# Performance work log

Measured on AMD Instinct MI355X. Metric: run time of the kernel, lower is better.

## Reference

```python
import jax, jax.numpy as jnp
import numpy as np

N, E, NS = 50000, 1600000, 25000
IN, HID, HEADS, EDIM = 5, 32, 4, 1
NEG_SLOPE = 0.2


def _gat(x, src, dst, ea, W, a_s, a_d, We, a_e, b, heads, out_ch, concat, n_nodes):
    # PyG GATConv (eval mode, dropout off): shared lin for src/dst, edge features fused.
    h = (x @ W).reshape(-1, heads, out_ch)               # [N, H, C]
    s_src = (h * a_s).sum(-1)                            # [N, H]
    s_dst = (h * a_d).sum(-1)                            # [N, H]
    he = (ea @ We).reshape(-1, heads, out_ch)            # [Ef, H, C]
    s_e = (he * a_e).sum(-1)                             # [Ef, H]
    logits = jax.nn.leaky_relu(s_src[src] + s_dst[dst] + s_e, NEG_SLOPE)  # [Ef, H]
    m = jax.ops.segment_max(logits, dst, num_segments=n_nodes)
    num = jnp.exp(logits - m[dst])
    den = jax.ops.segment_sum(num, dst, num_segments=n_nodes)
    alpha = num / (den[dst] + 1e-16)                     # per-dst softmax
    out = jax.ops.segment_sum(alpha[:, :, None] * h[src], dst, num_segments=n_nodes)
    out = out.reshape(n_nodes, heads * out_ch) if concat else out.mean(axis=1)
    return out + b, alpha


def setup_inputs():
    key = jax.random.key(0)
    ks = jax.random.split(key, 24)
    r = lambda i, shape: jax.random.normal(ks[i], shape, dtype=jnp.float32) * 0.1
    return dict(
        x=jax.random.normal(ks[0], (N, IN), dtype=jnp.float32),
        edge_attr=jax.random.normal(ks[1], (E, EDIM), dtype=jnp.float32),
        W1=r(2, (IN, HEADS * HID)), att_src1=r(3, (HEADS, HID)), att_dst1=r(4, (HEADS, HID)),
        We1=r(5, (EDIM, HEADS * HID)), att_e1=r(6, (HEADS, HID)), b1=jnp.zeros((HEADS * HID,), jnp.float32),
        W2=r(7, (HEADS * HID, HID)), att_src2=r(8, (1, HID)), att_dst2=r(9, (1, HID)),
        We2=r(10, (EDIM, HID)), att_e2=r(11, (1, HID)), b2=jnp.zeros((HID,), jnp.float32),
        Wa=r(12, (HID, 1)), ba=jnp.zeros((1,), jnp.float32),
        cash=jnp.zeros((1,), jnp.float32),
        Wc=r(13, (HID, 1)), bc=jnp.zeros((1,), jnp.float32),
        edge_index=jax.random.randint(ks[14], (2, E), 0, N),
        stock_idx=jnp.sort(jax.random.randint(ks[15], (NS,), 0, N)),
        batch=jnp.zeros((N,), jnp.int32),
    )


def reference(x, edge_attr, W1, att_src1, att_dst1, We1, att_e1, b1,
              W2, att_src2, att_dst2, We2, att_e2, b2,
              Wa, ba, cash, Wc, bc, edge_index, stock_idx, batch):
    src, dst = edge_index[0], edge_index[1]
    # add_self_loops with fill_value='mean' for edge_attr (PyG GATConv default)
    loop = jnp.arange(N, dtype=src.dtype)
    src_f = jnp.concatenate([src, loop])
    dst_f = jnp.concatenate([dst, loop])
    ea_mean = edge_attr.mean(axis=0, keepdims=True)
    ea_f = jnp.concatenate([edge_attr, jnp.broadcast_to(ea_mean, (N, EDIM))], axis=0)

    h1, alpha1 = _gat(x, src_f, dst_f, ea_f, W1, att_src1, att_dst1, We1, att_e1, b1, HEADS, HID, True, N)
    h1 = jax.nn.elu(h1)
    h2, _ = _gat(h1, src_f, dst_f, ea_f, W2, att_src2, att_dst2, We2, att_e2, b2, 1, HID, False, N)
    h2 = jax.nn.elu(h2)

    scores = (h2 @ Wa + ba)[:, 0]                        # actor head, [N]
    final = jnp.concatenate([cash, scores[stock_idx]])   # [NS+1]
    weights = jax.nn.softmax(final, axis=0)

    cnt = jax.ops.segment_sum(jnp.ones((N,), h2.dtype), batch, num_segments=1)
    graph_embed = jax.ops.segment_sum(h2, batch, num_segments=1) / cnt[:, None]
    value = graph_embed @ Wc + bc                        # [1, 1]

    edge_index_full = jnp.stack([src_f, dst_f])
    return weights, value, edge_index_full, alpha1
```

## Files before the change

### kernel.cpp

```cpp
#include <hip/hip_runtime.h>
#include <hip/hip_fp16.h>
#include <math.h>

#define N_NODES 50000
#define N_EDGES 1600000
#define EF      (N_EDGES + N_NODES)
#define NSTK    25000
#define IN_DIM  5
#define HID     32
#define HEADS   4
#define NEG_SLOPE 0.2f

#define SCAN_T  1024
#define CHUNK   ((N_NODES + SCAN_T - 1) / SCAN_T)
#define JMAX    128

#define NB      256
#define NBIN32  (N_NODES / 2)
#define CHUNK_E ((EF + NB - 1) / NB)

#define OUT_W   0
#define OUT_V   (NSTK + 1)
#define OUT_EIF (NSTK + 2)
#define OUT_A1  (OUT_EIF + 2 * EF)

struct alignas(8) EPack { int s; float av; };

__device__ __forceinline__ float lrelu(float x) { return x > 0.f ? x : NEG_SLOPE * x; }
__device__ __forceinline__ float elu1(float x)  { return x > 0.f ? x : expf(x) - 1.f; }

__global__ __launch_bounds__(256) void hist_pass(const int* __restrict__ ei,
                                                 const float* __restrict__ ea,
                                                 unsigned int* __restrict__ part,
                                                 float* hdr) {
    __shared__ unsigned int cnt[NBIN32];
    int b = blockIdx.x, t = threadIdx.x;
    for (int i = t; i < NBIN32; i += 256) cnt[i] = 0;
    __syncthreads();
    int e0 = b * CHUNK_E, e1 = min(e0 + CHUNK_E, EF);
    float s = 0.f;
    for (int e = e0 + t; e < e1; e += 256) {
        int d;
        if (e < N_EDGES) { d = ei[N_EDGES + e]; s += ea[e]; }
        else d = e - N_EDGES;
        atomicAdd(&cnt[d >> 1], (d & 1) ? 0x10000u : 1u);
    }
    __syncthreads();
    for (int i = t; i < NBIN32; i += 256) part[(size_t)b * NBIN32 + i] = cnt[i];
    #pragma unroll
    for (int off = 1; off < 64; off <<= 1) s += __shfl_xor(s, off);
    if ((t & 63) == 0) atomicAdd(&hdr[0], s);
}

__global__ void rebase(unsigned int* __restrict__ part, int* __restrict__ deg) {
    int i = blockIdx.x * blockDim.x + threadIdx.x;
    if (i >= NBIN32) return;
    unsigned int run0 = 0, run1 = 0;
    for (int b = 0; b < NB; b++) {
        size_t idx = (size_t)b * NBIN32 + i;
        unsigned int v = part[idx];
        part[idx] = (run1 << 16) | run0;
        run0 += v & 0xffffu;
        run1 += v >> 16;
    }
    deg[2 * i]     = (int)run0;
    deg[2 * i + 1] = (int)run1;
}

__global__ void scan_scalar(const int* __restrict__ deg, int* __restrict__ rowoff,
                            const float* __restrict__ We1, const float* __restrict__ ae1,
                            const float* __restrict__ We2, const float* __restrict__ ae2,
                            float* hdr) {
    __shared__ int sums[SCAN_T];
    int t = threadIdx.x;

    if (t < 128) {
        float p = We1[t] * ae1[t];
        #pragma unroll
        for (int off = 1; off < 32; off <<= 1) p += __shfl_xor(p, off);
        if ((t & 31) == 0) hdr[1 + (t >> 5)] = p;
        if (t < 32) {
            float q = We2[t] * ae2[t];
            #pragma unroll
            for (int off = 1; off < 32; off <<= 1) q += __shfl_xor(q, off);
            if (t == 0) { hdr[5] = q; hdr[0] = hdr[0] / (float)N_EDGES; }
        }
    }

    int base = t * CHUNK;
    int local = 0;
    for (int i = 0; i < CHUNK; i++) {
        int idx = base + i;
        if (idx < N_NODES) local += deg[idx];
    }
    sums[t] = local;
    __syncthreads();
    #pragma unroll
    for (int off = 1; off < SCAN_T; off <<= 1) {
        int v = (t >= off) ? sums[t - off] : 0;
        __syncthreads();
        sums[t] += v;
        __syncthreads();
    }
    int run = sums[t] - local;
    if (t == 0) rowoff[0] = 0;
    for (int i = 0; i < CHUNK; i++) {
        int idx = base + i;
        if (idx < N_NODES) { run += deg[idx]; rowoff[idx + 1] = run; }
    }
}

__global__ __launch_bounds__(256) void fill_pack(const int* __restrict__ ei,
                                                 const float* __restrict__ ea,
                                                 const int* __restrict__ rowoff,
                                                 const unsigned int* __restrict__ part,
                                                 const float* __restrict__ hdr,
                                                 EPack* __restrict__ epack,
                                                 float* __restrict__ out_eif) {
    __shared__ unsigned int cnt[NBIN32];
    int b = blockIdx.x, t = threadIdx.x;
    for (int i = t; i < NBIN32; i += 256) cnt[i] = 0;
    __syncthreads();
    float ea_mean = hdr[0];
    const unsigned short* rel = (const unsigned short*)(part + (size_t)b * NBIN32);
    int e0 = b * CHUNK_E, e1 = min(e0 + CHUNK_E, EF);
    for (int e = e0 + t; e < e1; e += 256) {
        int s, d; float av;
        if (e < N_EDGES) { s = ei[e]; d = ei[N_EDGES + e]; av = ea[e]; }
        else             { s = d = e - N_EDGES;            av = ea_mean; }
        unsigned int old = atomicAdd(&cnt[d >> 1], (d & 1) ? 0x10000u : 1u);
        unsigned int local = (d & 1) ? (old >> 16) : (old & 0xffffu);
        int pos = rowoff[d] + (int)rel[d] + (int)local;
        EPack ep; ep.s = s; ep.av = av;
        epack[pos] = ep;
        out_eif[e]      = (float)s;
        out_eif[EF + e] = (float)d;
    }
}

__global__ void node_lin1(const float* __restrict__ x, const float* __restrict__ W1,
                          const float* __restrict__ as1, const float* __restrict__ ad1,
                          __half* __restrict__ h1pre, float* __restrict__ ssrc1,
                          float* __restrict__ sdst1) {
    int n = blockIdx.x, t = threadIdx.x;
    float hv = 0.f;
    #pragma unroll
    for (int k = 0; k < IN_DIM; k++) hv += x[n * IN_DIM + k] * W1[k * 128 + t];
    h1pre[n * 128 + t] = __float2half(hv);
    float a = hv * as1[t];
    float b = hv * ad1[t];
    #pragma unroll
    for (int off = 1; off < 32; off <<= 1) { a += __shfl_xor(a, off); b += __shfl_xor(b, off); }
    if ((t & 31) == 0) { ssrc1[n * 4 + (t >> 5)] = a; sdst1[n * 4 + (t >> 5)] = b; }
}

__global__ void l1_agg(const EPack* __restrict__ epack, const int* __restrict__ rowoff,
                       const float* __restrict__ ssrc1, const float* __restrict__ sdst1,
                       const __half* __restrict__ h1pre, const float* __restrict__ b1,
                       const float* __restrict__ hdr, float* __restrict__ minv,
                       float* __restrict__ h1) {
    __shared__ float lds_p[4][HEADS][JMAX + 4];
    int wid = threadIdx.x >> 6;
    int n = blockIdx.x * 4 + wid;
    if (n >= N_NODES) return;
    int lane = threadIdx.x & 63;
    int start = rowoff[n], deg = rowoff[n + 1] - start;
    int hl = lane & 3;
    float ce = hdr[1 + hl];
    float sd = sdst1[n * 4 + hl];

    float m = -1e30f;
    for (int k = lane; k < deg * 4; k += 64) {
        EPack ep = epack[start + (k >> 2)];
        m = fmaxf(m, lrelu(ssrc1[ep.s * 4 + hl] + sd + ep.av * ce));
    }
    #pragma unroll
    for (int off = 4; off < 64; off <<= 1) m = fmaxf(m, __shfl_xor(m, off));

    float den = 0.f;
    for (int k = lane; k < deg * 4; k += 64) {
        int j = k >> 2;
        EPack ep = epack[start + j];
        float pv = expf(lrelu(ssrc1[ep.s * 4 + hl] + sd + ep.av * ce) - m);
        den += pv;
        if (j < JMAX) lds_p[wid][hl][j] = pv;
    }
    #pragma unroll
    for (int off = 4; off < 64; off <<= 1) den += __shfl_xor(den, off);
    float inv = 1.f / (den + 1e-16f);

    {
        float mh = __shfl(m,  lane & 3);
        float ih = __shfl(inv, lane & 3);
        if (lane < 8) minv[n * 8 + lane] = (lane < 4) ? mh : ih;
    }

    __builtin_amdgcn_wave_barrier();

    int sub = lane & 15, el = lane >> 4;
    int h = sub >> 2;
    float invh = __shfl(inv, h);
    int jcap = deg < JMAX ? deg : JMAX;
    float acc[8];
    #pragma unroll
    for (int i = 0; i < 8; i++) acc[i] = 0.f;

    for (int j0 = 0; j0 < jcap; j0 += 4) {
        int j = j0 + el;
        float a = 0.f; int s = 0;
        if (j < jcap) { a = lds_p[wid][h][j] * invh; s = epack[start + j].s; }
        const uint4 rv = *(const uint4*)(h1pre + (size_t)s * 128 + sub * 8);
        const __half2* hp = (const __half2*)&rv;
        #pragma unroll
        for (int i = 0; i < 4; i++) {
            float2 f = __half22float2(hp[i]);
            acc[2 * i]     += a * f.x;
            acc[2 * i + 1] += a * f.y;
        }
    }
    if (deg > JMAX) {
        float mh = __shfl(m, h), sdh = __shfl(sd, h), ceh = __shfl(ce, h);
        for (int j0 = JMAX; j0 < deg; j0 += 4) {
            int j = j0 + el;
            float a = 0.f; int s = 0;
            if (j < deg) {
                EPack ep = epack[start + j];
                s = ep.s;
                a = expf(lrelu(ssrc1[s * 4 + h] + sdh + ep.av * ceh) - mh) * invh;
            }
            const uint4 rv = *(const uint4*)(h1pre + (size_t)s * 128 + sub * 8);
            const __half2* hp = (const __half2*)&rv;
            #pragma unroll
            for (int i = 0; i < 4; i++) {
                float2 f = __half22float2(hp[i]);
                acc[2 * i]     += a * f.x;
                acc[2 * i + 1] += a * f.y;
            }
        }
    }

    #pragma unroll
    for (int i = 0; i < 8; i++) {
        acc[i] += __shfl_xor(acc[i], 16);
        acc[i] += __shfl_xor(acc[i], 32);
    }
    if (lane < 16) {
        int c0 = lane * 8;
        float4 bb0 = *(const float4*)(b1 + c0);
        float4 bb1 = *(const float4*)(b1 + c0 + 4);
        float4 r0 = make_float4(elu1(acc[0] + bb0.x), elu1(acc[1] + bb0.y),
                                elu1(acc[2] + bb0.z), elu1(acc[3] + bb0.w));
        float4 r1 = make_float4(elu1(acc[4] + bb1.x), elu1(acc[5] + bb1.y),
                                elu1(acc[6] + bb1.z), elu1(acc[7] + bb1.w));
        *(float4*)(h1 + n * 128 + c0)     = r0;
        *(float4*)(h1 + n * 128 + c0 + 4) = r1;
    }
}

__global__ void alpha_write(const int* __restrict__ ei, const float* __restrict__ ea,
                            const float* __restrict__ ssrc1, const float* __restrict__ sdst1,
                            const float* __restrict__ minv, const float* __restrict__ hdr,
                            float* __restrict__ alpha_out) {
    float ea_mean = hdr[0];
    float ce0 = hdr[1], ce1 = hdr[2], ce2 = hdr[3], ce3 = hdr[4];
    for (int e = blockIdx.x * blockDim.x + threadIdx.x; e < EF; e += gridDim.x * blockDim.x) {
        int s, d; float av;
        if (e < N_EDGES) { s = ei[e]; d = ei[N_EDGES + e]; av = ea[e]; }
        else             { s = d = e - N_EDGES;            av = ea_mean; }
        float4 ss = *(const float4*)(ssrc1 + (size_t)s * 4);
        float4 dd = *(const float4*)(sdst1 + (size_t)d * 4);
        float4 mm = *(const float4*)(minv + (size_t)d * 8);
        float4 iv = *(const float4*)(minv + (size_t)d * 8 + 4);
        float a0 = expf(lrelu(ss.x + dd.x + av * ce0) - mm.x) * iv.x;
        float a1 = expf(lrelu(ss.y + dd.y + av * ce1) - mm.y) * iv.y;
        float a2 = expf(lrelu(ss.z + dd.z + av * ce2) - mm.z) * iv.z;
        float a3 = expf(lrelu(ss.w + dd.w + av * ce3) - mm.w) * iv.w;
        float2* ap = (float2*)(alpha_out + (size_t)e * 4);
        ap[0] = make_float2(a0, a1);
        ap[1] = make_float2(a2, a3);
    }
}

__global__ void node_lin2(const float* __restrict__ h1, const float* __restrict__ W2,
                          const float* __restrict__ as2, const float* __restrict__ ad2,
                          float* __restrict__ h2pre, float* __restrict__ ssrc2,
                          float* __restrict__ sdst2) {
    __shared__ float sh[128];
    __shared__ float red[128];
    int n = blockIdx.x, t = threadIdx.x;
    sh[t] = h1[n * 128 + t];
    __syncthreads();
    int c = t & 31, q = t >> 5;
    float p = 0.f;
    #pragma unroll
    for (int k = 0; k < 32; k++) p += sh[q * 32 + k] * W2[(q * 32 + k) * 32 + c];
    red[t] = p;
    __syncthreads();
    if (t < 32) {
        float hv = red[t] + red[t + 32] + red[t + 64] + red[t + 96];
        h2pre[n * 32 + t] = hv;
        float a = hv * as2[t], b = hv * ad2[t];
        #pragma unroll
        for (int off = 1; off < 32; off <<= 1) { a += __shfl_xor(a, off); b += __shfl_xor(b, off); }
        if (t == 0) { ssrc2[n] = a; sdst2[n] = b; }
    }
}

__global__ void l2_agg(const EPack* __restrict__ epack, const int* __restrict__ rowoff,
                       const float* __restrict__ ssrc2, const float* __restrict__ sdst2,
                       const float* __restrict__ h2pre, const float* __restrict__ b2,
                       const float* __restrict__ hdr, float* __restrict__ h2) {
    __shared__ float lds_q[4][JMAX + 4];
    int wid = threadIdx.x >> 6;
    int n = blockIdx.x * 4 + wid;
    if (n >= N_NODES) return;
    int lane = threadIdx.x & 63;
    int start = rowoff[n], deg = rowoff[n + 1] - start;
    float ce = hdr[5];
    float sd = sdst2[n];

    float m = -1e30f;
    for (int k = lane; k < deg; k += 64) {
        EPack ep = epack[start + k];
        m = fmaxf(m, lrelu(ssrc2[ep.s] + sd + ep.av * ce));
    }
    #pragma unroll
    for (int off = 1; off < 64; off <<= 1) m = fmaxf(m, __shfl_xor(m, off));

    float den = 0.f;
    for (int k = lane; k < deg; k += 64) {
        EPack ep = epack[start + k];
        float pv = expf(lrelu(ssrc2[ep.s] + sd + ep.av * ce) - m);
        den += pv;
        if (k < JMAX) lds_q[wid][k] = pv;
    }
    #pragma unroll
    for (int off = 1; off < 64; off <<= 1) den += __shfl_xor(den, off);
    float inv = 1.f / (den + 1e-16f);

    __builtin_amdgcn_wave_barrier();

    int sub = lane & 15, el = lane >> 4;
    int jcap = deg < JMAX ? deg : JMAX;
    float acc0 = 0.f, acc1 = 0.f;
    for (int j0 = 0; j0 < jcap; j0 += 4) {
        int j = j0 + el;
        float a = 0.f; int s = 0;
        if (j < jcap) { a = lds_q[wid][j] * inv; s = epack[start + j].s; }
        float2 f = *(const float2*)(h2pre + (size_t)s * 32 + sub * 2);
        acc0 += a * f.x;
        acc1 += a * f.y;
    }
    if (deg > JMAX) {
        for (int j0 = JMAX; j0 < deg; j0 += 4) {
            int j = j0 + el;
            float a = 0.f; int s = 0;
            if (j < deg) {
                EPack ep = epack[start + j];
                s = ep.s;
                a = expf(lrelu(ssrc2[s] + sd + ep.av * ce) - m) * inv;
            }
            float2 f = *(const float2*)(h2pre + (size_t)s * 32 + sub * 2);
            acc0 += a * f.x;
            acc1 += a * f.y;
        }
    }
    acc0 += __shfl_xor(acc0, 16); acc0 += __shfl_xor(acc0, 32);
    acc1 += __shfl_xor(acc1, 16); acc1 += __shfl_xor(acc1, 32);
    if (lane < 16) {
        float2 bb = *(const float2*)(b2 + lane * 2);
        *(float2*)(h2 + n * 32 + lane * 2) =
            make_float2(elu1(acc0 + bb.x), elu1(acc1 + bb.y));
    }
}

__global__ void scores_value(const float* __restrict__ h2, const float* __restrict__ Wa,
                             const float* __restrict__ ba, const float* __restrict__ Wc,
                             float* __restrict__ scores, float* hdr) {
    int n = blockIdx.x * blockDim.x + threadIdx.x;
    float vc = 0.f;
    if (n < N_NODES) {
        float va = 0.f;
        #pragma unroll
        for (int cidx = 0; cidx < 32; cidx++) {
            float hv = h2[n * 32 + cidx];
            va += hv * Wa[cidx];
            vc += hv * Wc[cidx];
        }
        scores[n] = va + ba[0];
    }
    #pragma unroll
    for (int off = 1; off < 64; off <<= 1) vc += __shfl_xor(vc, off);
    if ((threadIdx.x & 63) == 0) atomicAdd(&hdr[6], vc);
}

__global__ void softmax_w(const float* __restrict__ scores, const int* __restrict__ sidx,
                          const float* __restrict__ cash, const float* __restrict__ hdr,
                          const float* __restrict__ bc, float* __restrict__ out) {
    __shared__ float red[1024];
    int t = threadIdx.x;
    float m = -1e30f;
    for (int i = t; i < NSTK + 1; i += 1024) {
        float v = (i == 0) ? cash[0] : scores[sidx[i - 1]];
        m = fmaxf(m, v);
    }
    red[t] = m;
    __syncthreads();
    for (int s = 512; s > 0; s >>= 1) { if (t < s) red[t] = fmaxf(red[t], red[t + s]); __syncthreads(); }
    m = red[0];
    __syncthreads();
    float sum = 0.f;
    for (int i = t; i < NSTK + 1; i += 1024) {
        float v = (i == 0) ? cash[0] : scores[sidx[i - 1]];
        sum += expf(v - m);
    }
    red[t] = sum;
    __syncthreads();
    for (int s = 512; s > 0; s >>= 1) { if (t < s) red[t] += red[t + s]; __syncthreads(); }
    float inv = 1.f / red[0];
    for (int i = t; i < NSTK + 1; i += 1024) {
        float v = (i == 0) ? cash[0] : scores[sidx[i - 1]];
        out[OUT_W + i] = expf(v - m) * inv;
    }
    if (t == 0) out[OUT_V] = hdr[6] / (float)N_NODES + bc[0];
}

extern "C" void kernel_launch(void* const* d_in, const int* in_sizes, int n_in,
                              void* d_out, int out_size, void* d_ws, size_t ws_size,
                              hipStream_t stream) {
    const float* x    = (const float*)d_in[0];
    const float* ea   = (const float*)d_in[1];
    const float* W1   = (const float*)d_in[2];
    const float* as1  = (const float*)d_in[3];
    const float* ad1  = (const float*)d_in[4];
    const float* We1  = (const float*)d_in[5];
    const float* ae1  = (const float*)d_in[6];
    const float* b1   = (const float*)d_in[7];
    const float* W2   = (const float*)d_in[8];
    const float* as2  = (const float*)d_in[9];
    const float* ad2  = (const float*)d_in[10];
    const float* We2  = (const float*)d_in[11];
    const float* ae2  = (const float*)d_in[12];
    const float* b2   = (const float*)d_in[13];
    const float* Wa   = (const float*)d_in[14];
    const float* ba   = (const float*)d_in[15];
    const float* cash = (const float*)d_in[16];
    const float* Wc   = (const float*)d_in[17];
    const float* bc   = (const float*)d_in[18];
    const int*   ei   = (const int*)d_in[19];
    const int*   sidx = (const int*)d_in[20];

    char* w = (char*)d_ws;
    float* hdr    = (float*)w;
    int*   deg    = (int*)(w + 256);
    int*   rowoff = deg + N_NODES;
    EPack* epack  = (EPack*)(rowoff + N_NODES + 4);
    __half* h1pre = (__half*)(epack + EF);
    float* ssrc1  = (float*)(h1pre + N_NODES * 128);
    float* sdst1  = ssrc1 + N_NODES * 4;
    float* minv   = sdst1 + N_NODES * 4;
    float* h1     = minv + N_NODES * 8;
    unsigned int* part = (unsigned int*)h1;
    float* h2pre  = h1 + N_NODES * 128;
    float* ssrc2  = h2pre + N_NODES * 32;
    float* sdst2  = ssrc2 + N_NODES;
    float* h2     = sdst2 + N_NODES;
    float* scores = h2 + N_NODES * 32;

    float* out = (float*)d_out;

    hipMemsetAsync(hdr, 0, 256, stream);

    hist_pass<<<NB, 256, 0, stream>>>(ei, ea, part, hdr);
    rebase<<<(NBIN32 + 255) / 256, 256, 0, stream>>>(part, deg);
    scan_scalar<<<1, SCAN_T, 0, stream>>>(deg, rowoff, We1, ae1, We2, ae2, hdr);
    fill_pack<<<NB, 256, 0, stream>>>(ei, ea, rowoff, part, hdr, epack, out + OUT_EIF);

    node_lin1<<<N_NODES, 128, 0, stream>>>(x, W1, as1, ad1, h1pre, ssrc1, sdst1);
    l1_agg<<<(N_NODES + 3) / 4, 256, 0, stream>>>(epack, rowoff, ssrc1, sdst1, h1pre,
                                                  b1, hdr, minv, h1);
    alpha_write<<<2048, 256, 0, stream>>>(ei, ea, ssrc1, sdst1, minv, hdr, out + OUT_A1);
    node_lin2<<<N_NODES, 128, 0, stream>>>(h1, W2, as2, ad2, h2pre, ssrc2, sdst2);
    l2_agg<<<(N_NODES + 3) / 4, 256, 0, stream>>>(epack, rowoff, ssrc2, sdst2, h2pre,
                                                  b2, hdr, h2);
    scores_value<<<(N_NODES + 255) / 256, 256, 0, stream>>>(h2, Wa, ba, Wc, scores, hdr);
    softmax_w<<<1, 1024, 0, stream>>>(scores, sidx, cash, hdr, bc, out);
}
```

Measured before the change: 588.4 us.

## Fuse layer-2 linear into layer-1 aggregation and cache logits in LDS

The node_lin2 kernel is folded into the tail of l1_agg: each wave keeps its ELU'd h1 row in LDS and computes the 128x32 projection plus the layer-2 attention scores directly, so the full h1 buffer no longer has to be written and read back and one launch disappears. Separately, both aggregation kernels now store raw logits in LDS during the max pass and apply exp from LDS in the denominator pass. This avoids re-gathering edge packs and source scores for the first JMAX edges. The cost is more per-wave work and LDS use in l1_agg, and W2 is read from global memory by every wave, which may lower occupancy.

Result: faster. 547.6 us (-6.9%).

```diff
diff --git a/kernel.cpp b/kernel.cpp
--- a/kernel.cpp
+++ b/kernel.cpp
@@ -157,9 +157,12 @@
 __global__ void l1_agg(const EPack* __restrict__ epack, const int* __restrict__ rowoff,
                        const float* __restrict__ ssrc1, const float* __restrict__ sdst1,
                        const __half* __restrict__ h1pre, const float* __restrict__ b1,
-                       const float* __restrict__ hdr, float* __restrict__ minv,
-                       float* __restrict__ h1) {
+                       const float* __restrict__ W2, const float* __restrict__ as2,
+                       const float* __restrict__ ad2, const float* __restrict__ hdr,
+                       float* __restrict__ minv, float* __restrict__ h2pre,
+                       float* __restrict__ ssrc2, float* __restrict__ sdst2) {
     __shared__ float lds_p[4][HEADS][JMAX + 4];
+    __shared__ float lds_h[4][132];
     int wid = threadIdx.x >> 6;
     int n = blockIdx.x * 4 + wid;
     if (n >= N_NODES) return;
@@ -168,22 +171,32 @@
     int hl = lane & 3;
     float ce = hdr[1 + hl];
     float sd = sdst1[n * 4 + hl];
+    int jcap = deg < JMAX ? deg : JMAX;
 
     float m = -1e30f;
-    for (int k = lane; k < deg * 4; k += 64) {
-        EPack ep = epack[start + (k >> 2)];
-        m = fmaxf(m, lrelu(ssrc1[ep.s * 4 + hl] + sd + ep.av * ce));
-    }
-    #pragma unroll
-    for (int off = 4; off < 64; off <<= 1) m = fmaxf(m, __shfl_xor(m, off));
-
-    float den = 0.f;
     for (int k = lane; k < deg * 4; k += 64) {
         int j = k >> 2;
         EPack ep = epack[start + j];
-        float pv = expf(lrelu(ssrc1[ep.s * 4 + hl] + sd + ep.av * ce) - m);
+        float lg = lrelu(ssrc1[ep.s * 4 + hl] + sd + ep.av * ce);
+        m = fmaxf(m, lg);
+        if (j < JMAX) lds_p[wid][hl][j] = lg;
+    }
+    #pragma unroll
+    for (int off = 4; off < 64; off <<= 1) m = fmaxf(m, __shfl_xor(m, off));
+
+    float den = 0.f;
+    for (int k = lane; k < jcap * 4; k += 64) {
+        int j = k >> 2;
+        float pv = expf(lds_p[wid][hl][j] - m);
+        lds_p[wid][hl][j] = pv;
         den += pv;
-        if (j < JMAX) lds_p[wid][hl][j] = pv;
+    }
+    if (deg > JMAX) {
+        for (int k = JMAX * 4 + lane; k < deg * 4; k += 64) {
+            int j = k >> 2;
+            EPack ep = epack[start + j];
+            den += expf(lrelu(ssrc1[ep.s * 4 + hl] + sd + ep.av * ce) - m);
+        }
     }
     #pragma unroll
     for (int off = 4; off < 64; off <<= 1) den += __shfl_xor(den, off);
@@ -200,7 +213,6 @@
     int sub = lane & 15, el = lane >> 4;
     int h = sub >> 2;
     float invh = __shfl(inv, h);
-    int jcap = deg < JMAX ? deg : JMAX;
     float acc[8];
     #pragma unroll
     for (int i = 0; i < 8; i++) acc[i] = 0.f;
@@ -252,9 +264,27 @@
                                 elu1(acc[2] + bb0.z), elu1(acc[3] + bb0.w));
         float4 r1 = make_float4(elu1(acc[4] + bb1.x), elu1(acc[5] + bb1.y),
                                 elu1(acc[6] + bb1.z), elu1(acc[7] + bb1.w));
-        *(float4*)(h1 + n * 128 + c0)     = r0;
-        *(float4*)(h1 + n * 128 + c0 + 4) = r1;
-    }
+        *(float4*)(&lds_h[wid][c0])     = r0;
+        *(float4*)(&lds_h[wid][c0 + 4]) = r1;
+    }
+    __builtin_amdgcn_wave_barrier();
+
+    int c = lane & 31, half = lane >> 5;
+    float acc2 = 0.f;
+    int kbase = half * 64;
+    #pragma unroll 8
+    for (int k = 0; k < 64; k++)
+        acc2 += lds_h[wid][kbase + k] * W2[(kbase + k) * 32 + c];
+    acc2 += __shfl_xor(acc2, 32);
+    float a2 = acc2 * as2[c];
+    float d2 = acc2 * ad2[c];
+    #pragma unroll
+    for (int off = 1; off < 32; off <<= 1) {
+        a2 += __shfl_xor(a2, off);
+        d2 += __shfl_xor(d2, off);
+    }
+    if (lane < 32) h2pre[n * 32 + c] = acc2;
+    if (lane == 0) { ssrc2[n] = a2; sdst2[n] = d2; }
 }
 
 __global__ void alpha_write(const int* __restrict__ ei, const float* __restrict__ ea,
@@ -281,31 +311,6 @@
     }
 }
 
-__global__ void node_lin2(const float* __restrict__ h1, const float* __restrict__ W2,
-                          const float* __restrict__ as2, const float* __restrict__ ad2,
-                          float* __restrict__ h2pre, float* __restrict__ ssrc2,
-                          float* __restrict__ sdst2) {
-    __shared__ float sh[128];
-    __shared__ float red[128];
-    int n = blockIdx.x, t = threadIdx.x;
-    sh[t] = h1[n * 128 + t];
-    __syncthreads();
-    int c = t & 31, q = t >> 5;
-    float p = 0.f;
-    #pragma unroll
-    for (int k = 0; k < 32; k++) p += sh[q * 32 + k] * W2[(q * 32 + k) * 32 + c];
-    red[t] = p;
-    __syncthreads();
-    if (t < 32) {
-        float hv = red[t] + red[t + 32] + red[t + 64] + red[t + 96];
-        h2pre[n * 32 + t] = hv;
-        float a = hv * as2[t], b = hv * ad2[t];
-        #pragma unroll
-        for (int off = 1; off < 32; off <<= 1) { a += __shfl_xor(a, off); b += __shfl_xor(b, off); }
-        if (t == 0) { ssrc2[n] = a; sdst2[n] = b; }
-    }
-}
-
 __global__ void l2_agg(const EPack* __restrict__ epack, const int* __restrict__ rowoff,
                        const float* __restrict__ ssrc2, const float* __restrict__ sdst2,
                        const float* __restrict__ h2pre, const float* __restrict__ b2,
@@ -318,21 +323,29 @@
     int start = rowoff[n], deg = rowoff[n + 1] - start;
     float ce = hdr[5];
     float sd = sdst2[n];
+    int jcap = deg < JMAX ? deg : JMAX;
 
     float m = -1e30f;
     for (int k = lane; k < deg; k += 64) {
         EPack ep = epack[start + k];
-        m = fmaxf(m, lrelu(ssrc2[ep.s] + sd + ep.av * ce));
+        float lg = lrelu(ssrc2[ep.s] + sd + ep.av * ce);
+        m = fmaxf(m, lg);
+        if (k < JMAX) lds_q[wid][k] = lg;
     }
     #pragma unroll
     for (int off = 1; off < 64; off <<= 1) m = fmaxf(m, __shfl_xor(m, off));
 
     float den = 0.f;
-    for (int k = lane; k < deg; k += 64) {
-        EPack ep = epack[start + k];
-        float pv = expf(lrelu(ssrc2[ep.s] + sd + ep.av * ce) - m);
+    for (int k = lane; k < jcap; k += 64) {
+        float pv = expf(lds_q[wid][k] - m);
+        lds_q[wid][k] = pv;
         den += pv;
-        if (k < JMAX) lds_q[wid][k] = pv;
+    }
+    if (deg > JMAX) {
+        for (int k = JMAX + lane; k < deg; k += 64) {
+            EPack ep = epack[start + k];
+            den += expf(lrelu(ssrc2[ep.s] + sd + ep.av * ce) - m);
+        }
     }
     #pragma unroll
     for (int off = 1; off < 64; off <<= 1) den += __shfl_xor(den, off);
@@ -341,7 +354,6 @@
     __builtin_amdgcn_wave_barrier();
 
     int sub = lane & 15, el = lane >> 4;
-    int jcap = deg < JMAX ? deg : JMAX;
     float acc0 = 0.f, acc1 = 0.f;
     for (int j0 = 0; j0 < jcap; j0 += 4) {
         int j = j0 + el;
@@ -459,9 +471,8 @@
     float* ssrc1  = (float*)(h1pre + N_NODES * 128);
     float* sdst1  = ssrc1 + N_NODES * 4;
     float* minv   = sdst1 + N_NODES * 4;
-    float* h1     = minv + N_NODES * 8;
-    unsigned int* part = (unsigned int*)h1;
-    float* h2pre  = h1 + N_NODES * 128;
+    unsigned int* part = (unsigned int*)(minv + N_NODES * 8);
+    float* h2pre  = (float*)(part + (size_t)NB * NBIN32);
     float* ssrc2  = h2pre + N_NODES * 32;
     float* sdst2  = ssrc2 + N_NODES;
     float* h2     = sdst2 + N_NODES;
@@ -478,9 +489,9 @@
 
     node_lin1<<<N_NODES, 128, 0, stream>>>(x, W1, as1, ad1, h1pre, ssrc1, sdst1);
     l1_agg<<<(N_NODES + 3) / 4, 256, 0, stream>>>(epack, rowoff, ssrc1, sdst1, h1pre,
-                                                  b1, hdr, minv, h1);
+                                                  b1, W2, as2, ad2, hdr, minv,
+                                                  h2pre, ssrc2, sdst2);
     alpha_write<<<2048, 256, 0, stream>>>(ei, ea, ssrc1, sdst1, minv, hdr, out + OUT_A1);
-    node_lin2<<<N_NODES, 128, 0, stream>>>(h1, W2, as2, ad2, h2pre, ssrc2, sdst2);
     l2_agg<<<(N_NODES + 3) / 4, 256, 0, stream>>>(epack, rowoff, ssrc2, sdst2, h2pre,
                                                   b2, hdr, h2);
     scores_value<<<(N_NODES + 255) / 256, 256, 0, stream>>>(h2, Wa, ba, Wc, scores, hdr);
```
